# Optimization experiments

Hardware: AMD Instinct MI355X
Metric: run time of the kernel (lower is better)

## Reference

```python
import jax, jax.numpy as jnp
import numpy as np

LATENT_DIM = 128
KQ_DIM = 32
B, N, K = 8, 16384, 16


def setup_inputs() -> dict:
    key = jax.random.key(0)
    k1, k2, k3, k4, k5, k6 = jax.random.split(key, 6)
    features = jax.random.normal(k1, (B, N, LATENT_DIM), dtype=jnp.float32)
    ks_w = jax.random.normal(k2, (KQ_DIM, LATENT_DIM), dtype=jnp.float32) * (LATENT_DIM ** -0.5)
    ks_b = jax.random.normal(k3, (KQ_DIM,), dtype=jnp.float32) * 0.01
    qs_w = jax.random.normal(k4, (KQ_DIM, LATENT_DIM), dtype=jnp.float32) * (LATENT_DIM ** -0.5)
    qs_b = jax.random.normal(k5, (KQ_DIM,), dtype=jnp.float32) * 0.01
    indices = jax.random.randint(k6, (3, B, N, K), 0, N, dtype=jnp.int64)
    return {"features": features, "ks_w": ks_w, "ks_b": ks_b,
            "qs_w": qs_w, "qs_b": qs_b, "indices": indices}


def reference(features, ks_w, ks_b, qs_w, qs_b, indices):
    # features: [B, N, latent_dim]; indices: [3, B, N, K]
    b, n, _ = features.shape
    k = indices.shape[-1]
    # Linear projections (torch Linear: x @ W^T + b)
    flatten_ks = jnp.einsum('bnl,dl->bnd', features, ks_w) + ks_b  # [B,N,D]
    flatten_qs = jnp.einsum('bnl,dl->bnd', features, qs_w) + qs_b  # [B,N,D]
    d = flatten_ks.shape[-1]
    # gather along node dim N using index channels 1 (x) and 2 (y)
    x_idx = indices[1].reshape(b, n * k)  # [B, N*K]
    y_idx = indices[2].reshape(b, n * k)
    x_features = jnp.take_along_axis(flatten_ks, x_idx[..., None], axis=1).reshape(b, n, k, d)
    y_features = jnp.take_along_axis(flatten_qs, y_idx[..., None], axis=1).reshape(b, n, k, d)
    # scaled dot-product affinity
    logits = jnp.sum(x_features * y_features, axis=-1) * (d ** -0.5)  # [B,N,K]
    return logits
```

## Files before the change

kernel.cpp:

```cpp
#include <hip/hip_runtime.h>

#define BATCH   8
#define NNODES  16384
#define KNBR    16
#define LATENT  128
#define DOUT    32
#define NROWS   (BATCH * NNODES)

typedef __attribute__((ext_vector_type(8))) short short8;
typedef __attribute__((ext_vector_type(4))) float floatx4;

__device__ __forceinline__ unsigned short f2bf(float f) {
    unsigned u = __float_as_uint(f);
    u += 0x7fff + ((u >> 16) & 1);
    return (unsigned short)(u >> 16);
}

__device__ __forceinline__ float dot2bf(unsigned a, unsigned b) {
    float alo = __uint_as_float(a << 16);
    float ahi = __uint_as_float(a & 0xffff0000u);
    float blo = __uint_as_float(b << 16);
    float bhi = __uint_as_float(b & 0xffff0000u);
    return alo * blo + ahi * bhi;
}

__device__ __forceinline__ void gload_lds16(const float* g, void* l) {
    __builtin_amdgcn_global_load_lds(
        (const __attribute__((address_space(1))) void*)g,
        (__attribute__((address_space(3))) void*)l,
        16, 0, 0);
}

#define BPAD 136

__global__ __launch_bounds__(256) void proj_kernel(
    const float* __restrict__ feats,
    const float* __restrict__ kw, const float* __restrict__ kb,
    const float* __restrict__ qw, const float* __restrict__ qb,
    unsigned short* __restrict__ tkb, unsigned short* __restrict__ tqb)
{
    __shared__ __align__(16) unsigned char A_raw[128 * 256];
    __shared__ unsigned short B_lds[64 * BPAD];
    __shared__ float bias_lds[64];

    const int tid  = threadIdx.x;
    const int lane = tid & 63;
    const int w    = tid >> 6;
    const int bat  = blockIdx.x & 7;
    const int u    = blockIdx.x >> 3;
    const long long blk_row = (long long)bat * NNODES + (long long)u * 128;

    {
        const float4* kw4 = (const float4*)kw;
        const float4* qw4 = (const float4*)qw;
#pragma unroll
        for (int i = 0; i < 8; ++i) {
            const int linear = i * 256 + tid;
            const int row = linear >> 5;
            const int c4  = linear & 31;
            const float4 v = (row < 32) ? kw4[row * 32 + c4] : qw4[(row - 32) * 32 + c4];
            unsigned lo = f2bf(v.x) | ((unsigned)f2bf(v.y) << 16);
            unsigned hi = f2bf(v.z) | ((unsigned)f2bf(v.w) << 16);
            *(uint2*)&B_lds[row * BPAD + c4 * 4] = make_uint2(lo, hi);
        }
        if (tid < 64) bias_lds[tid] = (tid < 32) ? kb[tid] : qb[tid - 32];
    }

    const int m = lane & 15;
    const int q = lane >> 4;

    floatx4 acc[2][4];
#pragma unroll
    for (int rt = 0; rt < 2; ++rt)
#pragma unroll
        for (int ct = 0; ct < 4; ++ct) acc[rt][ct] = (floatx4){0.f, 0.f, 0.f, 0.f};

    for (int ch = 0; ch < 2; ++ch) {
        if (ch) __syncthreads();

#pragma unroll
        for (int i = 0; i < 8; ++i) {
            const int L  = i * 4096 + tid * 16;
            const int r  = L >> 8;
            const int c0 = (((L & 255) ^ ((r & 7) << 4)) >> 2);
            gload_lds16(feats + (blk_row + r) * 128 + ch * 64 + c0, A_raw + L);
        }
        __syncthreads();

#pragma unroll
        for (int ks = 0; ks < 2; ++ks) {
            const int kg = ch * 64 + ks * 32 + q * 8;
            short8 bf[4];
#pragma unroll
            for (int ct = 0; ct < 4; ++ct)
                bf[ct] = *(const short8*)&B_lds[(ct * 16 + m) * BPAD + kg];
#pragma unroll
            for (int rt = 0; rt < 2; ++rt) {
                const int rloc = w * 32 + rt * 16 + m;
                const int b0   = rloc * 256 + ks * 128 + q * 32;
                const int p0   = b0 ^ ((rloc & 7) << 4);
                const float4 a0 = *(const float4*)(A_raw + p0);
                const float4 a1 = *(const float4*)(A_raw + (p0 ^ 16));
                union { short8 s; unsigned uu[4]; } af;
                af.uu[0] = f2bf(a0.x) | ((unsigned)f2bf(a0.y) << 16);
                af.uu[1] = f2bf(a0.z) | ((unsigned)f2bf(a0.w) << 16);
                af.uu[2] = f2bf(a1.x) | ((unsigned)f2bf(a1.y) << 16);
                af.uu[3] = f2bf(a1.z) | ((unsigned)f2bf(a1.w) << 16);
#pragma unroll
                for (int ct = 0; ct < 4; ++ct)
                    acc[rt][ct] = __builtin_amdgcn_mfma_f32_16x16x32_bf16(af.s, bf[ct], acc[rt][ct], 0, 0, 0);
            }
        }
    }

#pragma unroll
    for (int rt = 0; rt < 2; ++rt) {
#pragma unroll
        for (int reg = 0; reg < 4; ++reg) {
            const long long row = blk_row + w * 32 + rt * 16 + q * 4 + reg;
#pragma unroll
            for (int ct = 0; ct < 4; ++ct) {
                const float val = acc[rt][ct][reg] + bias_lds[ct * 16 + m];
                if (ct < 2) tkb[row * DOUT + ct * 16 + m]       = f2bf(val);
                else        tqb[row * DOUT + (ct - 2) * 16 + m] = f2bf(val);
            }
        }
    }
}

__global__ __launch_bounds__(256) void gather_dot_kernel(
    const unsigned short* __restrict__ tkb, const unsigned short* __restrict__ tqb,
    const int* __restrict__ idx, float* __restrict__ out)
{
    const long long NK  = (long long)NNODES * KNBR;
    const long long BNK = NK * BATCH;

    const int bat = blockIdx.x & 7;
    const int blk = blockIdx.x >> 3;
    const int tid = threadIdx.x;

    const uint4* tb_k = (const uint4*)(tkb + (long long)bat * NNODES * DOUT);
    const uint4* tb_q = (const uint4*)(tqb + (long long)bat * NNODES * DOUT);

#pragma unroll
    for (int p = 0; p < 4; ++p) {
        const long long local = (long long)blk * 1024 + p * 256 + tid;
        const long long o     = (long long)bat * NK + local;

        const int xi = __builtin_nontemporal_load(&idx[BNK + o]);
        const int yi = __builtin_nontemporal_load(&idx[2 * BNK + o]);

        const uint4* xr = tb_k + (long long)xi * 4;
        const uint4* yr = tb_q + (long long)yi * 4;
        const uint4 x0 = xr[0], x1 = xr[1], x2 = xr[2], x3 = xr[3];
        const uint4 y0 = yr[0], y1 = yr[1], y2 = yr[2], y3 = yr[3];

        float s = dot2bf(x0.x, y0.x) + dot2bf(x0.y, y0.y)
                + dot2bf(x0.z, y0.z) + dot2bf(x0.w, y0.w)
                + dot2bf(x1.x, y1.x) + dot2bf(x1.y, y1.y)
                + dot2bf(x1.z, y1.z) + dot2bf(x1.w, y1.w)
                + dot2bf(x2.x, y2.x) + dot2bf(x2.y, y2.y)
                + dot2bf(x2.z, y2.z) + dot2bf(x2.w, y2.w)
                + dot2bf(x3.x, y3.x) + dot2bf(x3.y, y3.y)
                + dot2bf(x3.z, y3.z) + dot2bf(x3.w, y3.w);

        __builtin_nontemporal_store(s * 0.17677669529663687f, &out[o]);
    }
}

extern "C" void kernel_launch(void* const* d_in, const int* in_sizes, int n_in,
                              void* d_out, int out_size, void* d_ws, size_t ws_size,
                              hipStream_t stream)
{
    const float* feats = (const float*)d_in[0];
    const float* kw    = (const float*)d_in[1];
    const float* kb    = (const float*)d_in[2];
    const float* qw    = (const float*)d_in[3];
    const float* qb    = (const float*)d_in[4];
    const int*   idx   = (const int*)d_in[5];
    float*       out   = (float*)d_out;

    unsigned short* tkb = (unsigned short*)d_ws;
    unsigned short* tqb = tkb + (long long)NROWS * DOUT;

    proj_kernel<<<NROWS / 128, 256, 0, stream>>>(feats, kw, kb, qw, qb, tkb, tqb);
    gather_dot_kernel<<<(int)((long long)BATCH * NNODES * KNBR / 1024), 256, 0, stream>>>(
        tkb, tqb, idx, out);
}
```

Measured before the change: 163.9 us.

## Split each gathered row across four lanes with shuffle reduction

Each output is now computed by a group of four lanes. Indices are loaded once per lane and broadcast within the quad by shuffles, and each lane gathers one 16-byte chunk of the key and query rows. Partial dot products are combined with xor shuffles, and the grid grows by four times so there is one output per thread. The aim is more coalesced gather loads (64 contiguous bytes per quad) and more memory parallelism, at the cost of extra shuffle instructions and more blocks.

Result: faster. 144.0 us (-12.2%).

```diff
diff --git a/kernel.cpp b/kernel.cpp
--- a/kernel.cpp
+++ b/kernel.cpp
@@ -135,37 +135,38 @@
     const long long NK  = (long long)NNODES * KNBR;
     const long long BNK = NK * BATCH;
 
-    const int bat = blockIdx.x & 7;
-    const int blk = blockIdx.x >> 3;
-    const int tid = threadIdx.x;
+    const int bat  = blockIdx.x & 7;
+    const int blk  = blockIdx.x >> 3;
+    const int tid  = threadIdx.x;
+    const int lane = tid & 63;
+    const int j    = tid & 3;
 
     const uint4* tb_k = (const uint4*)(tkb + (long long)bat * NNODES * DOUT);
     const uint4* tb_q = (const uint4*)(tqb + (long long)bat * NNODES * DOUT);
 
+    const long long o0 = (long long)bat * NK + (long long)blk * 256 + tid;
+
+    const int xi = __builtin_nontemporal_load(&idx[BNK + o0]);
+    const int yi = __builtin_nontemporal_load(&idx[2 * BNK + o0]);
+
+    float r0, r1, r2, r3;
 #pragma unroll
     for (int p = 0; p < 4; ++p) {
-        const long long local = (long long)blk * 1024 + p * 256 + tid;
-        const long long o     = (long long)bat * NK + local;
-
-        const int xi = __builtin_nontemporal_load(&idx[BNK + o]);
-        const int yi = __builtin_nontemporal_load(&idx[2 * BNK + o]);
-
-        const uint4* xr = tb_k + (long long)xi * 4;
-        const uint4* yr = tb_q + (long long)yi * 4;
-        const uint4 x0 = xr[0], x1 = xr[1], x2 = xr[2], x3 = xr[3];
-        const uint4 y0 = yr[0], y1 = yr[1], y2 = yr[2], y3 = yr[3];
-
-        float s = dot2bf(x0.x, y0.x) + dot2bf(x0.y, y0.y)
-                + dot2bf(x0.z, y0.z) + dot2bf(x0.w, y0.w)
-                + dot2bf(x1.x, y1.x) + dot2bf(x1.y, y1.y)
-                + dot2bf(x1.z, y1.z) + dot2bf(x1.w, y1.w)
-                + dot2bf(x2.x, y2.x) + dot2bf(x2.y, y2.y)
-                + dot2bf(x2.z, y2.z) + dot2bf(x2.w, y2.w)
-                + dot2bf(x3.x, y3.x) + dot2bf(x3.y, y3.y)
-                + dot2bf(x3.z, y3.z) + dot2bf(x3.w, y3.w);
-
-        __builtin_nontemporal_store(s * 0.17677669529663687f, &out[o]);
+        const int xp = __shfl(xi, (lane & ~3) | p);
+        const int yp = __shfl(yi, (lane & ~3) | p);
+        const uint4 x = tb_k[(long long)xp * 4 + j];
+        const uint4 y = tb_q[(long long)yp * 4 + j];
+        float s = dot2bf(x.x, y.x) + dot2bf(x.y, y.y)
+                + dot2bf(x.z, y.z) + dot2bf(x.w, y.w);
+        s += __shfl_xor(s, 1);
+        s += __shfl_xor(s, 2);
+        if      (p == 0) r0 = s;
+        else if (p == 1) r1 = s;
+        else if (p == 2) r2 = s;
+        else             r3 = s;
     }
+    const float v = (j == 0) ? r0 : (j == 1) ? r1 : (j == 2) ? r2 : r3;
+    __builtin_nontemporal_store(v * 0.17677669529663687f, &out[o0]);
 }
 
 extern "C" void kernel_launch(void* const* d_in, const int* in_sizes, int n_in,
@@ -184,6 +185,6 @@
     unsigned short* tqb = tkb + (long long)NROWS * DOUT;
 
     proj_kernel<<<NROWS / 128, 256, 0, stream>>>(feats, kw, kb, qw, qb, tkb, tqb);
-    gather_dot_kernel<<<(int)((long long)BATCH * NNODES * KNBR / 1024), 256, 0, stream>>>(
+    gather_dot_kernel<<<(int)((long long)BATCH * NNODES * KNBR / 256), 256, 0, stream>>>(
         tkb, tqb, idx, out);
 }
```
